# Optimization experiments

Measured on AMD Instinct MI355X. Metric: run time of the kernel, lower is better.

The kernel has to match this reference:

```python
import jax, jax.numpy as jnp
import numpy as np

N_NODES = 50000
N_EDGES = 800000
D_FEAT = 64
UNITS = 128  # concat=True -> each kernel maps D_FEAT -> UNITS//2


def setup_inputs() -> dict:
    key = jax.random.key(0)
    k1, k2, k3, k4, k5 = jax.random.split(key, 5)
    x = jax.random.normal(k1, (N_NODES, D_FEAT), dtype=jnp.float32)
    edge_index = jax.random.randint(k2, (2, N_EDGES), 0, N_NODES, dtype=jnp.int64)
    edge_weight = jax.random.uniform(k3, (N_EDGES,), dtype=jnp.float32)
    glorot = np.sqrt(6.0 / (D_FEAT + UNITS // 2)).astype(np.float32)
    self_kernel = jax.random.uniform(k4, (D_FEAT, UNITS // 2), dtype=jnp.float32, minval=-glorot, maxval=glorot)
    neighbor_kernel = jax.random.uniform(k5, (D_FEAT, UNITS // 2), dtype=jnp.float32, minval=-glorot, maxval=glorot)
    bias = jnp.zeros((UNITS,), dtype=jnp.float32)
    return {"x": x, "edge_index": edge_index, "edge_weight": edge_weight,
            "self_kernel": self_kernel, "neighbor_kernel": neighbor_kernel, "bias": bias}


def reference(x, edge_index, edge_weight, self_kernel, neighbor_kernel, bias):
    num_nodes = x.shape[0]
    row, col = edge_index[0], edge_index[1]  # row: target node, col: source neighbor
    # gather neighbor features and apply edge weights
    neighbor_x = x[col] * edge_weight[:, None]  # [E, D]
    # segment-mean over incoming edges of each target node
    sums = jax.ops.segment_sum(neighbor_x, row, num_segments=num_nodes)  # [N, D]
    counts = jax.ops.segment_sum(jnp.ones_like(edge_weight), row, num_segments=num_nodes)  # [N]
    neighbor_mean = sums / jnp.maximum(counts, 1.0)[:, None]
    # dual projection + concat (concat=True)
    from_self = x @ self_kernel              # [N, UNITS//2]
    from_neigh = neighbor_mean @ neighbor_kernel  # [N, UNITS//2]
    h = jnp.concatenate([from_self, from_neigh], axis=1) + bias
    h = jax.nn.relu(h)
    # normalize=False -> no l2 normalize
    return h
```

## Files before the change

kernel.cpp:

```cpp
#include <hip/hip_runtime.h>


typedef unsigned long long ull;
typedef __attribute__((ext_vector_type(8))) short bf16x8;
typedef __attribute__((ext_vector_type(4))) float f32x4;

constexpr int N_NODES = 50000;
constexpr int N_EDGES = 800000;
constexpr int D = 64;
constexpr int UNITS = 128;
constexpr int NB = (N_NODES + 255) / 256;
constexpr int SC_EPT = 16;
constexpr int SC_THREADS = 256;
constexpr int SC_CHUNK = SC_EPT * SC_THREADS;
constexpr int SC_BLOCKS = (N_EDGES + SC_CHUNK - 1) / SC_CHUNK;
constexpr int NS_THREADS = 256;
constexpr int NS_EPT = 24;
constexpr int PREP_BLOCKS = 2048;
constexpr int NTILES = N_NODES / 16;
constexpr int PJ_BLOCKS = (NTILES + 3) / 4;

__device__ __forceinline__ unsigned f2bf(float f) {
    unsigned u = __float_as_uint(f);
    return (u + 0x7fffu + ((u >> 16) & 1u)) >> 16;
}
__device__ __forceinline__ float bf2f(unsigned b) {
    return __uint_as_float(b << 16);
}

__global__ __launch_bounds__(256) void prep(const float* __restrict__ x,
                                            unsigned* __restrict__ xh,
                                            const int* __restrict__ ei,
                                            int* __restrict__ partial) {
    constexpr int XW = N_NODES * (D / 2);
    for (int i = blockIdx.x * 256 + threadIdx.x; i < XW; i += PREP_BLOCKS * 256) {
        const float2 v = ((const float2*)x)[i];
        xh[i] = f2bf(v.x) | (f2bf(v.y) << 16);
    }
    if (blockIdx.x < SC_BLOCKS) {
        __shared__ int lh[NB];
        for (int i = threadIdx.x; i < NB; i += 256) lh[i] = 0;
        __syncthreads();
        const int e0 = blockIdx.x * SC_CHUNK + threadIdx.x;
        #pragma unroll
        for (int i = 0; i < SC_EPT; ++i) {
            int e = e0 + i * SC_THREADS;
            if (e < N_EDGES) atomicAdd(&lh[ei[e] >> 8], 1);
        }
        __syncthreads();
        int* row = partial + (size_t)blockIdx.x * NB;
        for (int i = threadIdx.x; i < NB; i += 256) row[i] = lh[i];
    }
}

__global__ __launch_bounds__(256) void scan_cols(int* __restrict__ partial,
                                                 int* __restrict__ btot) {
    __shared__ int s[256];
    const int b = blockIdx.x;
    const int t = threadIdx.x;
    const int v = (t < SC_BLOCKS) ? partial[(size_t)t * NB + b] : 0;
    s[t] = v;
    __syncthreads();
    for (int d2 = 1; d2 < 256; d2 <<= 1) {
        int u = (t >= d2) ? s[t - d2] : 0;
        __syncthreads();
        s[t] += u;
        __syncthreads();
    }
    if (t < SC_BLOCKS) partial[(size_t)t * NB + b] = s[t] - v;
    if (t == 255) btot[b] = s[255];
}

__global__ __launch_bounds__(SC_THREADS) void edge_scatter(const int* __restrict__ ei,
                                                           const float* __restrict__ ew,
                                                           const int* __restrict__ partial,
                                                           const int* __restrict__ btot,
                                                           ull* __restrict__ packed) {
    __shared__ int sb[256];
    __shared__ int lbase[NB];
    __shared__ int lcur[NB];
    const int t = threadIdx.x;
    const int bv = (t < NB) ? btot[t] : 0;
    sb[t] = bv;
    __syncthreads();
    for (int d2 = 1; d2 < 256; d2 <<= 1) {
        int u = (t >= d2) ? sb[t - d2] : 0;
        __syncthreads();
        sb[t] += u;
        __syncthreads();
    }
    const int* row = partial + (size_t)blockIdx.x * NB;
    if (t < NB) {
        lbase[t] = (sb[t] - bv) + row[t];
        lcur[t]  = 0;
    }
    __syncthreads();
    const int e0 = blockIdx.x * SC_CHUNK + t;
    #pragma unroll
    for (int i = 0; i < SC_EPT; ++i) {
        const int e = e0 + i * SC_THREADS;
        if (e < N_EDGES) {
            const int   r = ei[e];
            const int   c = ei[N_EDGES + e];
            const float w = ew[e];
            const int   b = r >> 8;
            const int   lpos = atomicAdd(&lcur[b], 1);
            const unsigned hi = (unsigned)c | ((unsigned)(r & 255) << 16);
            packed[lbase[b] + lpos] = ((ull)hi << 32) | (ull)(unsigned)__float_as_uint(w);
        }
    }
}

__global__ __launch_bounds__(NS_THREADS) void node_sort(const int* __restrict__ btot,
                                                        int* __restrict__ offs,
                                                        const ull* __restrict__ packed,
                                                        unsigned* __restrict__ cedges) {
    __shared__ int cur[256];
    __shared__ int sc[256];
    __shared__ int sBase, sEnd;
    const int b = blockIdx.x;
    const int t = threadIdx.x;

    const int bv = (t < NB) ? btot[t] : 0;
    sc[t] = bv;
    __syncthreads();
    for (int d2 = 1; d2 < 256; d2 <<= 1) {
        int u = (t >= d2) ? sc[t - d2] : 0;
        __syncthreads();
        sc[t] += u;
        __syncthreads();
    }
    if (t == b) { sBase = sc[t] - bv; sEnd = sc[t]; }
    __syncthreads();
    const int s = sBase;
    const int e = sEnd;

    ull st[NS_EPT];
    #pragma unroll
    for (int i = 0; i < NS_EPT; ++i) {
        const int idx = s + t + i * NS_THREADS;
        st[i] = (idx < e) ? packed[idx] : ~0ull;
    }
    cur[t] = 0;
    __syncthreads();
    #pragma unroll
    for (int i = 0; i < NS_EPT; ++i) {
        if (st[i] != ~0ull) atomicAdd(&cur[(int)((st[i] >> 48) & 0xff)], 1);
    }
    __syncthreads();
    const int v = cur[t];
    sc[t] = v;
    __syncthreads();
    for (int d2 = 1; d2 < 256; d2 <<= 1) {
        int u = (t >= d2) ? sc[t - d2] : 0;
        __syncthreads();
        sc[t] += u;
        __syncthreads();
    }
    const int excl = sc[t] - v;
    const int n = b * 256 + t;
    if (n < N_NODES) offs[n] = s + excl;
    if (b == 0 && t == 0) offs[N_NODES] = N_EDGES;
    cur[t] = excl;
    __syncthreads();
    #pragma unroll
    for (int i = 0; i < NS_EPT; ++i) {
        if (st[i] != ~0ull) {
            const int r8  = (int)((st[i] >> 48) & 0xff);
            const int pos = atomicAdd(&cur[r8], 1);
            const unsigned hi  = (unsigned)(st[i] >> 32);
            const unsigned col = hi & 0xffffu;
            const unsigned wbf = f2bf(__uint_as_float((unsigned)st[i]));
            cedges[s + pos] = (col << 16) | wbf;
        }
    }
}

__global__ __launch_bounds__(256) void sage_aggregate(const unsigned* __restrict__ xh,
                                                      const int* __restrict__ offs,
                                                      const unsigned* __restrict__ cedges,
                                                      unsigned* __restrict__ meanh) {
    const int n = (blockIdx.x * 256 + threadIdx.x) >> 5;
    if (n >= N_NODES) return;
    const int l32 = threadIdx.x & 31;
    const int eg  = l32 >> 3;
    const int wq  = l32 & 7;
    const int s = offs[n];
    const int t = offs[n + 1];

    float ax0 = 0.f, ay0 = 0.f, ax1 = 0.f, ay1 = 0.f;
    float ax2 = 0.f, ay2 = 0.f, ax3 = 0.f, ay3 = 0.f;
    float bx0 = 0.f, by0 = 0.f, bx1 = 0.f, by1 = 0.f;
    float bx2 = 0.f, by2 = 0.f, bx3 = 0.f, by3 = 0.f;

    if (t > s) {
        const int tm1 = t - 1;
        for (int g = s; g < t; g += 8) {
            const int eA = g + eg;
            const int eB = g + 4 + eg;
            const unsigned cA = cedges[min(eA, tm1)];
            const unsigned cB = cedges[min(eB, tm1)];
            const float wA = (eA < t) ? bf2f(cA & 0xffffu) : 0.0f;
            const float wB = (eB < t) ? bf2f(cB & 0xffffu) : 0.0f;
            const uint4 vA = *(const uint4*)(xh + (size_t)(cA >> 16) * (D / 2) + wq * 4);
            const uint4 vB = *(const uint4*)(xh + (size_t)(cB >> 16) * (D / 2) + wq * 4);
            ax0 = fmaf(__uint_as_float(vA.x << 16),         wA, ax0);
            ay0 = fmaf(__uint_as_float(vA.x & 0xffff0000u), wA, ay0);
            ax1 = fmaf(__uint_as_float(vA.y << 16),         wA, ax1);
            ay1 = fmaf(__uint_as_float(vA.y & 0xffff0000u), wA, ay1);
            ax2 = fmaf(__uint_as_float(vA.z << 16),         wA, ax2);
            ay2 = fmaf(__uint_as_float(vA.z & 0xffff0000u), wA, ay2);
            ax3 = fmaf(__uint_as_float(vA.w << 16),         wA, ax3);
            ay3 = fmaf(__uint_as_float(vA.w & 0xffff0000u), wA, ay3);
            bx0 = fmaf(__uint_as_float(vB.x << 16),         wB, bx0);
            by0 = fmaf(__uint_as_float(vB.x & 0xffff0000u), wB, by0);
            bx1 = fmaf(__uint_as_float(vB.y << 16),         wB, bx1);
            by1 = fmaf(__uint_as_float(vB.y & 0xffff0000u), wB, by1);
            bx2 = fmaf(__uint_as_float(vB.z << 16),         wB, bx2);
            by2 = fmaf(__uint_as_float(vB.z & 0xffff0000u), wB, by2);
            bx3 = fmaf(__uint_as_float(vB.w << 16),         wB, bx3);
            by3 = fmaf(__uint_as_float(vB.w & 0xffff0000u), wB, by3);
        }
    }
    float sx0 = ax0 + bx0, sy0 = ay0 + by0;
    float sx1 = ax1 + bx1, sy1 = ay1 + by1;
    float sx2 = ax2 + bx2, sy2 = ay2 + by2;
    float sx3 = ax3 + bx3, sy3 = ay3 + by3;
    sx0 += __shfl_xor(sx0, 8);  sx0 += __shfl_xor(sx0, 16);
    sy0 += __shfl_xor(sy0, 8);  sy0 += __shfl_xor(sy0, 16);
    sx1 += __shfl_xor(sx1, 8);  sx1 += __shfl_xor(sx1, 16);
    sy1 += __shfl_xor(sy1, 8);  sy1 += __shfl_xor(sy1, 16);
    sx2 += __shfl_xor(sx2, 8);  sx2 += __shfl_xor(sx2, 16);
    sy2 += __shfl_xor(sy2, 8);  sy2 += __shfl_xor(sy2, 16);
    sx3 += __shfl_xor(sx3, 8);  sx3 += __shfl_xor(sx3, 16);
    sy3 += __shfl_xor(sy3, 8);  sy3 += __shfl_xor(sy3, 16);

    if (eg == 0) {
        const float inv = 1.0f / fmaxf((float)(t - s), 1.0f);
        uint4 r;
        r.x = f2bf(sx0 * inv) | (f2bf(sy0 * inv) << 16);
        r.y = f2bf(sx1 * inv) | (f2bf(sy1 * inv) << 16);
        r.z = f2bf(sx2 * inv) | (f2bf(sy2 * inv) << 16);
        r.w = f2bf(sx3 * inv) | (f2bf(sy3 * inv) << 16);
        *(uint4*)(meanh + (size_t)n * (D / 2) + wq * 4) = r;
    }
}

__global__ __launch_bounds__(256) void sage_project(const unsigned* __restrict__ xh,
                                                    const unsigned* __restrict__ meanh,
                                                    const float* __restrict__ skern,
                                                    const float* __restrict__ nkern,
                                                    const float* __restrict__ bias,
                                                    float* __restrict__ out) {
    const int lane = threadIdx.x & 63;
    const int wid  = (blockIdx.x * 256 + threadIdx.x) >> 6;
    const int r16  = lane & 15;
    const int g    = lane >> 4;

    bf16x8 bfrag[16];
    #pragma unroll
    for (int ct = 0; ct < 8; ++ct) {
        const float* K = (ct < 4) ? skern : nkern;
        const int col = (ct & 3) * 16 + r16;
        #pragma unroll
        for (int kh = 0; kh < 2; ++kh) {
            bf16x8 f;
            #pragma unroll
            for (int j = 0; j < 8; ++j) {
                const int k = kh * 32 + 8 * g + j;
                f[j] = (short)f2bf(K[k * 64 + col]);
            }
            bfrag[ct * 2 + kh] = f;
        }
    }

    if (wid >= NTILES) return;
    const int n0 = wid * 16;

    const unsigned* xrow = xh    + (size_t)(n0 + r16) * (D / 2);
    const unsigned* mrow = meanh + (size_t)(n0 + r16) * (D / 2);
    const bf16x8 aS0 = *(const bf16x8*)(xrow + 4 * g);
    const bf16x8 aS1 = *(const bf16x8*)(xrow + 16 + 4 * g);
    const bf16x8 aN0 = *(const bf16x8*)(mrow + 4 * g);
    const bf16x8 aN1 = *(const bf16x8*)(mrow + 16 + 4 * g);

    f32x4 acc[8];
    #pragma unroll
    for (int ct = 0; ct < 8; ++ct) {
        f32x4 c = {0.f, 0.f, 0.f, 0.f};
        c = __builtin_amdgcn_mfma_f32_16x16x32_bf16(ct < 4 ? aS0 : aN0, bfrag[ct * 2 + 0], c, 0, 0, 0);
        c = __builtin_amdgcn_mfma_f32_16x16x32_bf16(ct < 4 ? aS1 : aN1, bfrag[ct * 2 + 1], c, 0, 0, 0);
        acc[ct] = c;
    }

    #pragma unroll
    for (int ct = 0; ct < 8; ++ct) {
        const int col = (ct < 4 ? 0 : 64) + (ct & 3) * 16 + r16;
        const float bj = bias[col];
        #pragma unroll
        for (int r = 0; r < 4; ++r) {
            const int node = n0 + 4 * g + r;
            out[(size_t)node * UNITS + col] = fmaxf(acc[ct][r] + bj, 0.0f);
        }
    }
}

extern "C" void kernel_launch(void* const* d_in, const int* in_sizes, int n_in,
                              void* d_out, int out_size, void* d_ws, size_t ws_size,
                              hipStream_t stream) {
    const float* x     = (const float*)d_in[0];
    const int*   ei    = (const int*)  d_in[1];
    const float* ew    = (const float*)d_in[2];
    const float* skern = (const float*)d_in[3];
    const float* nkern = (const float*)d_in[4];
    const float* bias  = (const float*)d_in[5];
    float* out = (float*)d_out;

    auto align256 = [](size_t v) { return (v + 255) & ~size_t(255); };
    const size_t szM  = align256((size_t)SC_BLOCKS * NB * sizeof(int));
    const size_t szT  = align256((size_t)NB * sizeof(int));
    const size_t szNO = align256((size_t)(N_NODES + 1) * sizeof(int));
    const size_t szP  = align256((size_t)N_EDGES * sizeof(ull));
    const size_t szC  = align256((size_t)N_EDGES * sizeof(unsigned));
    const size_t szX  = align256((size_t)N_NODES * (D / 2) * sizeof(unsigned));

    char* w = (char*)d_ws;
    int*      partial = (int*)w;
    int*      btot    = (int*)(w + szM);
    int*      offs    = (int*)(w + szM + szT);
    ull*      packed  = (ull*)(w + szM + szT + szNO);
    unsigned* cedges  = (unsigned*)(w + szM + szT + szNO + szP);
    unsigned* xh      = (unsigned*)(w + szM + szT + szNO + szP + szC);
    unsigned* meanh   = (unsigned*)(w + szM + szT + szNO + szP + szC + szX);
    (void)ws_size; (void)in_sizes; (void)n_in; (void)out_size;

    prep          <<<PREP_BLOCKS, 256, 0, stream>>>(x, xh, ei, partial);
    scan_cols     <<<NB, 256, 0, stream>>>(partial, btot);
    edge_scatter  <<<SC_BLOCKS, SC_THREADS, 0, stream>>>(ei, ew, partial, btot, packed);
    node_sort     <<<NB, NS_THREADS, 0, stream>>>(btot, offs, packed, cedges);
    sage_aggregate<<<(N_NODES * 32 + 255) / 256, 256, 0, stream>>>(xh, offs, cedges, meanh);
    sage_project  <<<PJ_BLOCKS, 256, 0, stream>>>(xh, meanh, skern, nkern, bias, out);
}
```

Before: 64.73 us.

## Fuse CSR build kernels into one persistent kernel with grid barriers

```diff
diff --git a/kernel.cpp b/kernel.cpp
--- a/kernel.cpp
+++ b/kernel.cpp
@@ -14,7 +14,6 @@
 constexpr int SC_THREADS = 256;
 constexpr int SC_CHUNK = SC_EPT * SC_THREADS;
 constexpr int SC_BLOCKS = (N_EDGES + SC_CHUNK - 1) / SC_CHUNK;
-constexpr int NS_THREADS = 256;
 constexpr int NS_EPT = 24;
 constexpr int PREP_BLOCKS = 2048;
 constexpr int NTILES = N_NODES / 16;
@@ -28,150 +27,155 @@
     return __uint_as_float(b << 16);
 }
 
+__device__ __forceinline__ void gridbar(int* ctr, int target) {
+    __threadfence();
+    __syncthreads();
+    if (threadIdx.x == 0) {
+        __hip_atomic_fetch_add(ctr, 1, __ATOMIC_RELEASE, __HIP_MEMORY_SCOPE_AGENT);
+        while (__hip_atomic_load(ctr, __ATOMIC_ACQUIRE, __HIP_MEMORY_SCOPE_AGENT) < target) {
+            __builtin_amdgcn_s_sleep(8);
+        }
+    }
+    __syncthreads();
+    __threadfence();
+}
+
 __global__ __launch_bounds__(256) void prep(const float* __restrict__ x,
                                             unsigned* __restrict__ xh,
-                                            const int* __restrict__ ei,
-                                            int* __restrict__ partial) {
+                                            int* __restrict__ bar) {
+    if (blockIdx.x == 0 && threadIdx.x < 8) bar[threadIdx.x] = 0;
     constexpr int XW = N_NODES * (D / 2);
     for (int i = blockIdx.x * 256 + threadIdx.x; i < XW; i += PREP_BLOCKS * 256) {
         const float2 v = ((const float2*)x)[i];
         xh[i] = f2bf(v.x) | (f2bf(v.y) << 16);
     }
-    if (blockIdx.x < SC_BLOCKS) {
-        __shared__ int lh[NB];
-        for (int i = threadIdx.x; i < NB; i += 256) lh[i] = 0;
-        __syncthreads();
-        const int e0 = blockIdx.x * SC_CHUNK + threadIdx.x;
-        #pragma unroll
-        for (int i = 0; i < SC_EPT; ++i) {
-            int e = e0 + i * SC_THREADS;
-            if (e < N_EDGES) atomicAdd(&lh[ei[e] >> 8], 1);
-        }
-        __syncthreads();
-        int* row = partial + (size_t)blockIdx.x * NB;
-        for (int i = threadIdx.x; i < NB; i += 256) row[i] = lh[i];
-    }
-}
-
-__global__ __launch_bounds__(256) void scan_cols(int* __restrict__ partial,
-                                                 int* __restrict__ btot) {
-    __shared__ int s[256];
+}
+
+__global__ __launch_bounds__(256) void csr_build(const int* __restrict__ ei,
+                                                 const float* __restrict__ ew,
+                                                 int* __restrict__ partial,
+                                                 int* __restrict__ btot,
+                                                 int* __restrict__ bar,
+                                                 int* __restrict__ offs,
+                                                 ull* __restrict__ packed,
+                                                 unsigned* __restrict__ cedges) {
+    __shared__ int lh[NB];
+    __shared__ int lbase[NB];
+    __shared__ int sb[256];
+    __shared__ int bofs[NB + 1];
+    __shared__ int cur[256];
     const int b = blockIdx.x;
     const int t = threadIdx.x;
-    const int v = (t < SC_BLOCKS) ? partial[(size_t)t * NB + b] : 0;
-    s[t] = v;
-    __syncthreads();
-    for (int d2 = 1; d2 < 256; d2 <<= 1) {
-        int u = (t >= d2) ? s[t - d2] : 0;
-        __syncthreads();
-        s[t] += u;
-        __syncthreads();
-    }
-    if (t < SC_BLOCKS) partial[(size_t)t * NB + b] = s[t] - v;
-    if (t == 255) btot[b] = s[255];
-}
-
-__global__ __launch_bounds__(SC_THREADS) void edge_scatter(const int* __restrict__ ei,
-                                                           const float* __restrict__ ew,
-                                                           const int* __restrict__ partial,
-                                                           const int* __restrict__ btot,
-                                                           ull* __restrict__ packed) {
-    __shared__ int sb[256];
-    __shared__ int lbase[NB];
-    __shared__ int lcur[NB];
-    const int t = threadIdx.x;
-    const int bv = (t < NB) ? btot[t] : 0;
-    sb[t] = bv;
-    __syncthreads();
-    for (int d2 = 1; d2 < 256; d2 <<= 1) {
-        int u = (t >= d2) ? sb[t - d2] : 0;
-        __syncthreads();
-        sb[t] += u;
-        __syncthreads();
-    }
-    const int* row = partial + (size_t)blockIdx.x * NB;
-    if (t < NB) {
-        lbase[t] = (sb[t] - bv) + row[t];
-        lcur[t]  = 0;
-    }
-    __syncthreads();
-    const int e0 = blockIdx.x * SC_CHUNK + t;
+
+    int   rows[SC_EPT];
+    int   cols[SC_EPT];
+    float wts[SC_EPT];
+    for (int i = t; i < NB; i += 256) lh[i] = 0;
+    __syncthreads();
+    const int e0 = b * SC_CHUNK + t;
     #pragma unroll
     for (int i = 0; i < SC_EPT; ++i) {
         const int e = e0 + i * SC_THREADS;
         if (e < N_EDGES) {
-            const int   r = ei[e];
-            const int   c = ei[N_EDGES + e];
-            const float w = ew[e];
-            const int   b = r >> 8;
-            const int   lpos = atomicAdd(&lcur[b], 1);
-            const unsigned hi = (unsigned)c | ((unsigned)(r & 255) << 16);
-            packed[lbase[b] + lpos] = ((ull)hi << 32) | (ull)(unsigned)__float_as_uint(w);
-        }
-    }
-}
-
-__global__ __launch_bounds__(NS_THREADS) void node_sort(const int* __restrict__ btot,
-                                                        int* __restrict__ offs,
-                                                        const ull* __restrict__ packed,
-                                                        unsigned* __restrict__ cedges) {
-    __shared__ int cur[256];
-    __shared__ int sc[256];
-    __shared__ int sBase, sEnd;
-    const int b = blockIdx.x;
-    const int t = threadIdx.x;
-
-    const int bv = (t < NB) ? btot[t] : 0;
-    sc[t] = bv;
-    __syncthreads();
-    for (int d2 = 1; d2 < 256; d2 <<= 1) {
-        int u = (t >= d2) ? sc[t - d2] : 0;
-        __syncthreads();
-        sc[t] += u;
-        __syncthreads();
-    }
-    if (t == b) { sBase = sc[t] - bv; sEnd = sc[t]; }
-    __syncthreads();
-    const int s = sBase;
-    const int e = sEnd;
-
-    ull st[NS_EPT];
-    #pragma unroll
-    for (int i = 0; i < NS_EPT; ++i) {
-        const int idx = s + t + i * NS_THREADS;
-        st[i] = (idx < e) ? packed[idx] : ~0ull;
-    }
-    cur[t] = 0;
-    __syncthreads();
-    #pragma unroll
-    for (int i = 0; i < NS_EPT; ++i) {
-        if (st[i] != ~0ull) atomicAdd(&cur[(int)((st[i] >> 48) & 0xff)], 1);
-    }
-    __syncthreads();
-    const int v = cur[t];
-    sc[t] = v;
-    __syncthreads();
-    for (int d2 = 1; d2 < 256; d2 <<= 1) {
-        int u = (t >= d2) ? sc[t - d2] : 0;
-        __syncthreads();
-        sc[t] += u;
-        __syncthreads();
-    }
-    const int excl = sc[t] - v;
-    const int n = b * 256 + t;
-    if (n < N_NODES) offs[n] = s + excl;
-    if (b == 0 && t == 0) offs[N_NODES] = N_EDGES;
-    cur[t] = excl;
-    __syncthreads();
-    #pragma unroll
-    for (int i = 0; i < NS_EPT; ++i) {
-        if (st[i] != ~0ull) {
-            const int r8  = (int)((st[i] >> 48) & 0xff);
-            const int pos = atomicAdd(&cur[r8], 1);
-            const unsigned hi  = (unsigned)(st[i] >> 32);
-            const unsigned col = hi & 0xffffu;
-            const unsigned wbf = f2bf(__uint_as_float((unsigned)st[i]));
-            cedges[s + pos] = (col << 16) | wbf;
+            rows[i] = ei[e];
+            cols[i] = ei[N_EDGES + e];
+            wts[i]  = ew[e];
+            atomicAdd(&lh[rows[i] >> 8], 1);
+        } else {
+            rows[i] = -1;
+        }
+    }
+    __syncthreads();
+    for (int i = t; i < NB; i += 256) partial[(size_t)b * NB + i] = lh[i];
+    gridbar(bar + 0, NB);
+
+    {
+        const int v = (t < SC_BLOCKS) ? partial[(size_t)t * NB + b] : 0;
+        sb[t] = v;
+        __syncthreads();
+        for (int d2 = 1; d2 < 256; d2 <<= 1) {
+            int u = (t >= d2) ? sb[t - d2] : 0;
+            __syncthreads();
+            sb[t] += u;
+            __syncthreads();
+        }
+        if (t < SC_BLOCKS) partial[(size_t)t * NB + b] = sb[t] - v;
+        if (t == 255) btot[b] = sb[255];
+    }
+    gridbar(bar + 1, NB);
+
+    {
+        const int bv = (t < NB) ? btot[t] : 0;
+        sb[t] = bv;
+        __syncthreads();
+        for (int d2 = 1; d2 < 256; d2 <<= 1) {
+            int u = (t >= d2) ? sb[t - d2] : 0;
+            __syncthreads();
+            sb[t] += u;
+            __syncthreads();
+        }
+        if (t < NB) bofs[t] = sb[t] - bv;
+        if (t == 255) bofs[NB] = sb[255];
+        __syncthreads();
+        for (int i = t; i < NB; i += 256) {
+            lbase[i] = bofs[i] + partial[(size_t)b * NB + i];
+            lh[i]    = 0;
+        }
+    }
+    __syncthreads();
+
+    #pragma unroll
+    for (int i = 0; i < SC_EPT; ++i) {
+        if (rows[i] >= 0) {
+            const int bb   = rows[i] >> 8;
+            const int lpos = atomicAdd(&lh[bb], 1);
+            const unsigned hi = (unsigned)cols[i] | ((unsigned)(rows[i] & 255) << 16);
+            packed[lbase[bb] + lpos] = ((ull)hi << 32) | (ull)(unsigned)__float_as_uint(wts[i]);
+        }
+    }
+    gridbar(bar + 2, NB);
+
+    {
+        const int s = bofs[b];
+        const int e = bofs[b + 1];
+        ull st[NS_EPT];
+        #pragma unroll
+        for (int i = 0; i < NS_EPT; ++i) {
+            const int idx = s + t + i * 256;
+            st[i] = (idx < e) ? packed[idx] : ~0ull;
+        }
+        cur[t] = 0;
+        __syncthreads();
+        #pragma unroll
+        for (int i = 0; i < NS_EPT; ++i) {
+            if (st[i] != ~0ull) atomicAdd(&cur[(int)((st[i] >> 48) & 0xff)], 1);
+        }
+        __syncthreads();
+        const int v = cur[t];
+        sb[t] = v;
+        __syncthreads();
+        for (int d2 = 1; d2 < 256; d2 <<= 1) {
+            int u = (t >= d2) ? sb[t - d2] : 0;
+            __syncthreads();
+            sb[t] += u;
+            __syncthreads();
+        }
+        const int excl = sb[t] - v;
+        const int n = b * 256 + t;
+        if (n < N_NODES) offs[n] = s + excl;
+        if (b == 0 && t == 0) offs[N_NODES] = N_EDGES;
+        cur[t] = excl;
+        __syncthreads();
+        #pragma unroll
+        for (int i = 0; i < NS_EPT; ++i) {
+            if (st[i] != ~0ull) {
+                const int r8  = (int)((st[i] >> 48) & 0xff);
+                const int pos = atomicAdd(&cur[r8], 1);
+                const unsigned hi  = (unsigned)(st[i] >> 32);
+                const unsigned col = hi & 0xffffu;
+                const unsigned wbf = f2bf(__uint_as_float((unsigned)st[i]));
+                cedges[s + pos] = (col << 16) | wbf;
+            }
         }
     }
 }
@@ -319,6 +323,7 @@
     auto align256 = [](size_t v) { return (v + 255) & ~size_t(255); };
     const size_t szM  = align256((size_t)SC_BLOCKS * NB * sizeof(int));
     const size_t szT  = align256((size_t)NB * sizeof(int));
+    const size_t szB  = align256(8 * sizeof(int));
     const size_t szNO = align256((size_t)(N_NODES + 1) * sizeof(int));
     const size_t szP  = align256((size_t)N_EDGES * sizeof(ull));
     const size_t szC  = align256((size_t)N_EDGES * sizeof(unsigned));
@@ -327,17 +332,16 @@
     char* w = (char*)d_ws;
     int*      partial = (int*)w;
     int*      btot    = (int*)(w + szM);
-    int*      offs    = (int*)(w + szM + szT);
-    ull*      packed  = (ull*)(w + szM + szT + szNO);
-    unsigned* cedges  = (unsigned*)(w + szM + szT + szNO + szP);
-    unsigned* xh      = (unsigned*)(w + szM + szT + szNO + szP + szC);
-    unsigned* meanh   = (unsigned*)(w + szM + szT + szNO + szP + szC + szX);
+    int*      bar     = (int*)(w + szM + szT);
+    int*      offs    = (int*)(w + szM + szT + szB);
+    ull*      packed  = (ull*)(w + szM + szT + szB + szNO);
+    unsigned* cedges  = (unsigned*)(w + szM + szT + szB + szNO + szP);
+    unsigned* xh      = (unsigned*)(w + szM + szT + szB + szNO + szP + szC);
+    unsigned* meanh   = (unsigned*)(w + szM + szT + szB + szNO + szP + szC + szX);
     (void)ws_size; (void)in_sizes; (void)n_in; (void)out_size;
 
-    prep          <<<PREP_BLOCKS, 256, 0, stream>>>(x, xh, ei, partial);
-    scan_cols     <<<NB, 256, 0, stream>>>(partial, btot);
-    edge_scatter  <<<SC_BLOCKS, SC_THREADS, 0, stream>>>(ei, ew, partial, btot, packed);
-    node_sort     <<<NB, NS_THREADS, 0, stream>>>(btot, offs, packed, cedges);
+    prep          <<<PREP_BLOCKS, 256, 0, stream>>>(x, xh, bar);
+    csr_build     <<<NB, 256, 0, stream>>>(ei, ew, partial, btot, bar, offs, packed, cedges);
     sage_aggregate<<<(N_NODES * 32 + 255) / 256, 256, 0, stream>>>(xh, offs, cedges, meanh);
     sage_project  <<<PJ_BLOCKS, 256, 0, stream>>>(xh, meanh, skern, nkern, bias, out);
 }
```

Measured after the change: 191.8 us. 196% more time.
